# Kernel tuning notes

Hardware: AMD Instinct MI355X
Metric: run time of the kernel (lower is better)

## Reference

```python
import jax, jax.numpy as jnp
import numpy as np

NUM_SEGMENTS = 1024  # batch_size (graphs per batch)
NUM_HEADS = 4
HIDDEN = 64
INPUT_DIM = 512
NUM_NODES = 262144


def setup_inputs() -> dict:
    key = jax.random.key(0)
    ks = jax.random.split(key, 8)
    x = jax.random.normal(ks[0], (NUM_NODES, INPUT_DIM), dtype=jnp.float32)
    batch = jnp.sort(jax.random.randint(ks[1], (NUM_NODES,), 0, NUM_SEGMENTS)).astype(jnp.int64)
    # per-head attention projection weights/biases (torch Linear: y = x @ W.T + b)
    Wh = jax.random.normal(ks[2], (NUM_HEADS, HIDDEN, INPUT_DIM), dtype=jnp.float32) * 0.05
    bh = jnp.zeros((NUM_HEADS, HIDDEN), dtype=jnp.float32)
    ctx = jax.random.normal(ks[3], (NUM_HEADS, HIDDEN), dtype=jnp.float32) * 0.1
    Wc = jax.random.normal(ks[4], (INPUT_DIM, NUM_HEADS * INPUT_DIM), dtype=jnp.float32) * 0.02
    bc = jnp.zeros((INPUT_DIM,), dtype=jnp.float32)
    return {"x": x, "batch": batch, "Wh": Wh, "bh": bh, "ctx": ctx, "Wc": Wc, "bc": bc}


def _segment_softmax(scores, batch, num_segments):
    # scores: [N, H]; softmax over nodes within each graph segment, per head
    seg_max = jax.ops.segment_max(scores, batch, num_segments=num_segments)  # [B, H]
    shifted = jnp.exp(scores - seg_max[batch])                               # [N, H]
    seg_sum = jax.ops.segment_sum(shifted, batch, num_segments=num_segments)  # [B, H]
    return shifted / seg_sum[batch]


def reference(x, batch, Wh, bh, ctx, Wc, bc):
    batch = batch.astype(jnp.int32)
    # all heads at once: logits [N, H, K]
    logits = jnp.einsum('nd,hkd->nhk', x, Wh) + bh
    scores = jnp.einsum('nhk,hk->nh', jnp.tanh(logits), ctx)   # [N, H]
    weights = _segment_softmax(scores, batch, NUM_SEGMENTS)     # [N, H]
    weighted = weights[:, :, None] * x[:, None, :]              # [N, H, D]
    pooled = jax.ops.segment_sum(weighted, batch, num_segments=NUM_SEGMENTS)  # [B, H, D]
    concatenated = pooled.reshape(NUM_SEGMENTS, NUM_HEADS * INPUT_DIM)  # head0|head1|... order
    return concatenated @ Wc.T + bc
```

## Files before the change

### kernel.cpp

```cpp
#include <hip/hip_runtime.h>

#define NNODES 262144
#define NSEG   1024
#define DIN    512
#define NB     32
#define NBLK   (NNODES / NB)

typedef __attribute__((ext_vector_type(8))) short bf16x8;
typedef __attribute__((ext_vector_type(4))) float f32x4;

__device__ __forceinline__ unsigned short f2bf(float f){
  unsigned u = __float_as_uint(f);
  u += 0x7FFFu + ((u >> 16) & 1u);
  return (unsigned short)(u >> 16);
}

__device__ __forceinline__ float tanh_fast(float v){
  float z = fminf(fmaxf(v, -15.f), 15.f);
  float e = __expf(2.f * z);
  return (e - 1.f) / (e + 1.f);
}

__device__ __forceinline__ void atomic_addf(float* p, float v){
  __hip_atomic_fetch_add(p, v, __ATOMIC_RELAXED, __HIP_MEMORY_SCOPE_AGENT);
}

__global__ __launch_bounds__(256)
void k_prep(const float* __restrict__ wh, const float* __restrict__ wc,
            unsigned short* __restrict__ wbt, float* __restrict__ wct,
            float4* __restrict__ pooled4, float4* __restrict__ zsum4){
  int g = blockIdx.x * 256 + threadIdx.x;
  if (g < 131072){
    int ks = g >> 13, rem = g & 8191, hk = rem >> 5, kl = rem & 31;
    wbt[g] = f2bf(wh[hk * DIN + ks * 32 + kl]);
  } else if (g < 131072 + 1048576){
    int g2 = g - 131072;
    int j = g2 >> 9, o = g2 & 511;
    wct[g2] = wc[o * 2048 + j];
  } else if (g < 131072 + 1048576 + 524288){
    pooled4[g - 131072 - 1048576] = (float4){0.f, 0.f, 0.f, 0.f};
  } else if (g < 131072 + 1048576 + 524288 + 1024){
    zsum4[g - 131072 - 1048576 - 524288] = (float4){0.f, 0.f, 0.f, 0.f};
  }
}

__global__ __launch_bounds__(256)
void k_main(const float* __restrict__ x, const unsigned short* __restrict__ wbt,
            const float* __restrict__ bh, const float* __restrict__ ctx,
            const int* __restrict__ batch, float* __restrict__ pooled,
            float* __restrict__ zsum){
  __shared__ __align__(16) unsigned short xs[NB * DIN];
  __shared__ __align__(16) float wl[NB][4];
  __shared__ int bcache[NB];
  const int t = threadIdx.x, w = t >> 6, l = t & 63;
  const int nb = blockIdx.x * NB;

  const float4* xp = (const float4*)(x + (size_t)nb * DIN);
#pragma unroll 4
  for (int i = 0; i < 16; ++i){
    float4 v = xp[i * 256 + t];
    int flat = i * 1024 + t * 4;
    int row = flat >> 9, col = flat & 511;
    unsigned lo = (unsigned)f2bf(v.x) | ((unsigned)f2bf(v.y) << 16);
    unsigned hi = (unsigned)f2bf(v.z) | ((unsigned)f2bf(v.w) << 16);
    int byte = (row << 10) + (col << 1);
    byte ^= (row & 7) << 4;
    *(uint2*)((char*)xs + byte) = make_uint2(lo, hi);
  }
  if (t < NB) bcache[t] = batch[nb + t];

  float bhv[4], cxv[4];
#pragma unroll
  for (int q = 0; q < 4; ++q){
    int hk = (w * 4 + q) * 16 + (l & 15);
    bhv[q] = bh[hk];
    cxv[q] = ctx[hk];
  }

  bf16x8 Ba[4], Bb[4];
#pragma unroll
  for (int q = 0; q < 4; ++q)
    Ba[q] = *(const bf16x8*)(wbt + ((w * 4 + q) * 16 + (l & 15)) * 32 + (l >> 4) * 8);

  f32x4 acc[2][4];
#pragma unroll
  for (int nt = 0; nt < 2; ++nt)
#pragma unroll
    for (int q = 0; q < 4; ++q) acc[nt][q] = (f32x4){0.f, 0.f, 0.f, 0.f};

  __syncthreads();

  const int fr  = (l & 15);
  const int fcb = (l >> 4) * 16;
#pragma unroll
  for (int ks2 = 0; ks2 < 16; ks2 += 2){
    {
      const unsigned short* wp = wbt + (ks2 + 1) * 8192;
#pragma unroll
      for (int q = 0; q < 4; ++q)
        Bb[q] = *(const bf16x8*)(wp + ((w * 4 + q) * 16 + fr) * 32 + (l >> 4) * 8);
    }
    {
      int b0 = (fr << 10) + (ks2 << 6) + fcb;        b0 ^= (fr & 7) << 4;
      int b1 = ((16 + fr) << 10) + (ks2 << 6) + fcb; b1 ^= (fr & 7) << 4;
      bf16x8 A0 = *(const bf16x8*)((const char*)xs + b0);
      bf16x8 A1 = *(const bf16x8*)((const char*)xs + b1);
#pragma unroll
      for (int q = 0; q < 4; ++q){
        acc[0][q] = __builtin_amdgcn_mfma_f32_16x16x32_bf16(A0, Ba[q], acc[0][q], 0, 0, 0);
        acc[1][q] = __builtin_amdgcn_mfma_f32_16x16x32_bf16(A1, Ba[q], acc[1][q], 0, 0, 0);
      }
    }
    if (ks2 + 2 < 16){
      const unsigned short* wp = wbt + (ks2 + 2) * 8192;
#pragma unroll
      for (int q = 0; q < 4; ++q)
        Ba[q] = *(const bf16x8*)(wp + ((w * 4 + q) * 16 + fr) * 32 + (l >> 4) * 8);
    }
    {
      int b0 = (fr << 10) + ((ks2 + 1) << 6) + fcb;        b0 ^= (fr & 7) << 4;
      int b1 = ((16 + fr) << 10) + ((ks2 + 1) << 6) + fcb; b1 ^= (fr & 7) << 4;
      bf16x8 A0 = *(const bf16x8*)((const char*)xs + b0);
      bf16x8 A1 = *(const bf16x8*)((const char*)xs + b1);
#pragma unroll
      for (int q = 0; q < 4; ++q){
        acc[0][q] = __builtin_amdgcn_mfma_f32_16x16x32_bf16(A0, Bb[q], acc[0][q], 0, 0, 0);
        acc[1][q] = __builtin_amdgcn_mfma_f32_16x16x32_bf16(A1, Bb[q], acc[1][q], 0, 0, 0);
      }
    }
  }

#pragma unroll
  for (int r = 0; r < 4; ++r){
    float s0 = 0.f, s1 = 0.f;
#pragma unroll
    for (int q = 0; q < 4; ++q){
      s0 += tanh_fast(acc[0][q][r] + bhv[q]) * cxv[q];
      s1 += tanh_fast(acc[1][q][r] + bhv[q]) * cxv[q];
    }
#pragma unroll
    for (int off = 1; off < 16; off <<= 1){
      s0 += __shfl_xor(s0, off);
      s1 += __shfl_xor(s1, off);
    }
    if ((l & 15) == 0){
      int node0 = (l >> 4) * 4 + r;
      wl[node0][w]      = __expf(s0);
      wl[16 + node0][w] = __expf(s1);
    }
  }
  __syncthreads();

  float2 a0 = {0.f,0.f}, a1 = {0.f,0.f}, a2 = {0.f,0.f}, a3 = {0.f,0.f};
  int cur = bcache[0], run0 = 0;

#pragma unroll 4
  for (int n = 0; n < NB; ++n){
    int sg = bcache[n];
    if (sg != cur){
      float* base = pooled + (size_t)cur * 2048 + 2 * t;
      atomic_addf(base + 0,      a0.x); atomic_addf(base + 1,      a0.y);
      atomic_addf(base + 512,    a1.x); atomic_addf(base + 513,    a1.y);
      atomic_addf(base + 1024,   a2.x); atomic_addf(base + 1025,   a2.y);
      atomic_addf(base + 1536,   a3.x); atomic_addf(base + 1537,   a3.y);
      if (t < 4){
        float zs = 0.f;
        for (int m = run0; m < n; ++m) zs += wl[m][t];
        atomic_addf(zsum + cur * 4 + t, zs);
      }
      a0 = a1 = a2 = a3 = (float2){0.f, 0.f};
      cur = sg; run0 = n;
    }
    int byte = (n << 10) + (t << 2);
    byte ^= (n & 7) << 4;
    unsigned xv = *(const unsigned*)((const char*)xs + byte);
    float x0 = __uint_as_float(xv << 16);
    float x1 = __uint_as_float(xv & 0xFFFF0000u);
    float4 wv = *(const float4*)&wl[n][0];
    a0.x += wv.x * x0; a0.y += wv.x * x1;
    a1.x += wv.y * x0; a1.y += wv.y * x1;
    a2.x += wv.z * x0; a2.y += wv.z * x1;
    a3.x += wv.w * x0; a3.y += wv.w * x1;
  }
  {
    float* base = pooled + (size_t)cur * 2048 + 2 * t;
    atomic_addf(base + 0,      a0.x); atomic_addf(base + 1,      a0.y);
    atomic_addf(base + 512,    a1.x); atomic_addf(base + 513,    a1.y);
    atomic_addf(base + 1024,   a2.x); atomic_addf(base + 1025,   a2.y);
    atomic_addf(base + 1536,   a3.x); atomic_addf(base + 1537,   a3.y);
    if (t < 4){
      float zs = 0.f;
      for (int m = run0; m < NB; ++m) zs += wl[m][t];
      atomic_addf(zsum + cur * 4 + t, zs);
    }
  }
}

__global__ __launch_bounds__(256)
void k_out(const float* __restrict__ pooled, const float* __restrict__ wct,
           const float* __restrict__ zsum, const float* __restrict__ bias,
           float* __restrict__ out){
  __shared__ float ps[32][32];
  __shared__ float wt[32][64];
  __shared__ float rz[32][4];
  const int t = threadIdx.x;
  const int br = blockIdx.x >> 3, bc = blockIdx.x & 7;
  const int r0 = br * 32, c0 = bc * 64;
  if (t < 128){
    int row = t >> 2, h = t & 3;
    float z = zsum[(r0 + row) * 4 + h];
    rz[row][h] = (z > 0.f) ? 1.f / z : 0.f;
  }
  __syncthreads();

  const int w4 = t >> 6, col = t & 63;
  float acc[8];
#pragma unroll
  for (int i = 0; i < 8; ++i) acc[i] = 0.f;

  for (int j0 = 0; j0 < 2048; j0 += 32){
#pragma unroll
    for (int i = 0; i < 4; ++i){
      int e = i * 256 + t;
      int row = e >> 5, jj = e & 31;
      int j = j0 + jj;
      ps[row][jj] = pooled[(size_t)(r0 + row) * 2048 + j] * rz[row][j >> 9];
    }
#pragma unroll
    for (int i = 0; i < 8; ++i){
      int e = i * 256 + t;
      int jr = e >> 6, cc = e & 63;
      wt[jr][cc] = wct[(size_t)(j0 + jr) * 512 + c0 + cc];
    }
    __syncthreads();
#pragma unroll 8
    for (int jj = 0; jj < 32; ++jj){
      float wv = wt[jj][col];
#pragma unroll
      for (int i = 0; i < 8; ++i)
        acc[i] += ps[w4 * 8 + i][jj] * wv;
    }
    __syncthreads();
  }
  float bv = bias[c0 + col];
#pragma unroll
  for (int i = 0; i < 8; ++i)
    out[(size_t)(r0 + w4 * 8 + i) * 512 + c0 + col] = acc[i] + bv;
}

extern "C" void kernel_launch(void* const* d_in, const int* in_sizes, int n_in,
                              void* d_out, int out_size, void* d_ws, size_t ws_size,
                              hipStream_t stream){
  const float* x     = (const float*)d_in[0];
  const int*   batch = (const int*)d_in[1];
  const float* Wh    = (const float*)d_in[2];
  const float* bh    = (const float*)d_in[3];
  const float* ctx   = (const float*)d_in[4];
  const float* Wc    = (const float*)d_in[5];
  const float* bcv   = (const float*)d_in[6];
  float* out = (float*)d_out;

  char* ws = (char*)d_ws;
  unsigned short* wbt = (unsigned short*)(ws + 0);
  float* wct          = (float*)(ws + 262144);
  float* pooled       = (float*)(ws + 4456448);
  float* zsum         = (float*)(ws + 12845056);

  k_prep<<<6660, 256, 0, stream>>>(Wh, Wc, wbt, wct, (float4*)pooled, (float4*)zsum);
  k_main<<<NBLK, 256, 0, stream>>>(x, wbt, bh, ctx, batch, pooled, zsum);
  k_out <<<256, 256, 0, stream>>>(pooled, wct, zsum, bcv, out);
}
```

Baseline: 943.5 us.

## Double node tile per block, drop Wc transpose, shrink output tiles

```diff
diff --git a/kernel.cpp b/kernel.cpp
--- a/kernel.cpp
+++ b/kernel.cpp
@@ -3,7 +3,7 @@
 #define NNODES 262144
 #define NSEG   1024
 #define DIN    512
-#define NB     32
+#define NB     64
 #define NBLK   (NNODES / NB)
 
 typedef __attribute__((ext_vector_type(8))) short bf16x8;
@@ -26,21 +26,17 @@
 }
 
 __global__ __launch_bounds__(256)
-void k_prep(const float* __restrict__ wh, const float* __restrict__ wc,
-            unsigned short* __restrict__ wbt, float* __restrict__ wct,
+void k_prep(const float* __restrict__ wh,
+            unsigned short* __restrict__ wbt,
             float4* __restrict__ pooled4, float4* __restrict__ zsum4){
   int g = blockIdx.x * 256 + threadIdx.x;
   if (g < 131072){
     int ks = g >> 13, rem = g & 8191, hk = rem >> 5, kl = rem & 31;
     wbt[g] = f2bf(wh[hk * DIN + ks * 32 + kl]);
-  } else if (g < 131072 + 1048576){
-    int g2 = g - 131072;
-    int j = g2 >> 9, o = g2 & 511;
-    wct[g2] = wc[o * 2048 + j];
-  } else if (g < 131072 + 1048576 + 524288){
-    pooled4[g - 131072 - 1048576] = (float4){0.f, 0.f, 0.f, 0.f};
-  } else if (g < 131072 + 1048576 + 524288 + 1024){
-    zsum4[g - 131072 - 1048576 - 524288] = (float4){0.f, 0.f, 0.f, 0.f};
+  } else if (g < 131072 + 524288){
+    pooled4[g - 131072] = (float4){0.f, 0.f, 0.f, 0.f};
+  } else if (g < 131072 + 524288 + 1024){
+    zsum4[g - 131072 - 524288] = (float4){0.f, 0.f, 0.f, 0.f};
   }
 }
 
@@ -56,10 +52,10 @@
   const int nb = blockIdx.x * NB;
 
   const float4* xp = (const float4*)(x + (size_t)nb * DIN);
-#pragma unroll 4
-  for (int i = 0; i < 16; ++i){
+#pragma unroll 8
+  for (int i = 0; i < 32; ++i){
     float4 v = xp[i * 256 + t];
-    int flat = i * 1024 + t * 4;
+    int flat = (i * 256 + t) * 4;
     int row = flat >> 9, col = flat & 511;
     unsigned lo = (unsigned)f2bf(v.x) | ((unsigned)f2bf(v.y) << 16);
     unsigned hi = (unsigned)f2bf(v.z) | ((unsigned)f2bf(v.w) << 16);
@@ -69,10 +65,11 @@
   }
   if (t < NB) bcache[t] = batch[nb + t];
 
+  const int fr = l & 15, fc8 = (l >> 4) * 8;
   float bhv[4], cxv[4];
 #pragma unroll
   for (int q = 0; q < 4; ++q){
-    int hk = (w * 4 + q) * 16 + (l & 15);
+    int hk = (w * 4 + q) * 16 + fr;
     bhv[q] = bh[hk];
     cxv[q] = ctx[hk];
   }
@@ -80,17 +77,16 @@
   bf16x8 Ba[4], Bb[4];
 #pragma unroll
   for (int q = 0; q < 4; ++q)
-    Ba[q] = *(const bf16x8*)(wbt + ((w * 4 + q) * 16 + (l & 15)) * 32 + (l >> 4) * 8);
-
-  f32x4 acc[2][4];
-#pragma unroll
-  for (int nt = 0; nt < 2; ++nt)
+    Ba[q] = *(const bf16x8*)(wbt + ((w * 4 + q) * 16 + fr) * 32 + fc8);
+
+  f32x4 acc[4][4];
+#pragma unroll
+  for (int nt = 0; nt < 4; ++nt)
 #pragma unroll
     for (int q = 0; q < 4; ++q) acc[nt][q] = (f32x4){0.f, 0.f, 0.f, 0.f};
 
   __syncthreads();
 
-  const int fr  = (l & 15);
   const int fcb = (l >> 4) * 16;
 #pragma unroll
   for (int ks2 = 0; ks2 < 16; ks2 += 2){
@@ -98,55 +94,57 @@
       const unsigned short* wp = wbt + (ks2 + 1) * 8192;
 #pragma unroll
       for (int q = 0; q < 4; ++q)
-        Bb[q] = *(const bf16x8*)(wp + ((w * 4 + q) * 16 + fr) * 32 + (l >> 4) * 8);
+        Bb[q] = *(const bf16x8*)(wp + ((w * 4 + q) * 16 + fr) * 32 + fc8);
     }
     {
-      int b0 = (fr << 10) + (ks2 << 6) + fcb;        b0 ^= (fr & 7) << 4;
-      int b1 = ((16 + fr) << 10) + (ks2 << 6) + fcb; b1 ^= (fr & 7) << 4;
-      bf16x8 A0 = *(const bf16x8*)((const char*)xs + b0);
-      bf16x8 A1 = *(const bf16x8*)((const char*)xs + b1);
-#pragma unroll
-      for (int q = 0; q < 4; ++q){
-        acc[0][q] = __builtin_amdgcn_mfma_f32_16x16x32_bf16(A0, Ba[q], acc[0][q], 0, 0, 0);
-        acc[1][q] = __builtin_amdgcn_mfma_f32_16x16x32_bf16(A1, Ba[q], acc[1][q], 0, 0, 0);
+      bf16x8 A[4];
+#pragma unroll
+      for (int nt = 0; nt < 4; ++nt){
+        int b = ((nt * 16 + fr) << 10) + (ks2 << 6) + fcb;
+        b ^= (fr & 7) << 4;
+        A[nt] = *(const bf16x8*)((const char*)xs + b);
       }
+#pragma unroll
+      for (int nt = 0; nt < 4; ++nt)
+#pragma unroll
+        for (int q = 0; q < 4; ++q)
+          acc[nt][q] = __builtin_amdgcn_mfma_f32_16x16x32_bf16(A[nt], Ba[q], acc[nt][q], 0, 0, 0);
     }
     if (ks2 + 2 < 16){
       const unsigned short* wp = wbt + (ks2 + 2) * 8192;
 #pragma unroll
       for (int q = 0; q < 4; ++q)
-        Ba[q] = *(const bf16x8*)(wp + ((w * 4 + q) * 16 + fr) * 32 + (l >> 4) * 8);
+        Ba[q] = *(const bf16x8*)(wp + ((w * 4 + q) * 16 + fr) * 32 + fc8);
     }
     {
-      int b0 = (fr << 10) + ((ks2 + 1) << 6) + fcb;        b0 ^= (fr & 7) << 4;
-      int b1 = ((16 + fr) << 10) + ((ks2 + 1) << 6) + fcb; b1 ^= (fr & 7) << 4;
-      bf16x8 A0 = *(const bf16x8*)((const char*)xs + b0);
-      bf16x8 A1 = *(const bf16x8*)((const char*)xs + b1);
-#pragma unroll
-      for (int q = 0; q < 4; ++q){
-        acc[0][q] = __builtin_amdgcn_mfma_f32_16x16x32_bf16(A0, Bb[q], acc[0][q], 0, 0, 0);
-        acc[1][q] = __builtin_amdgcn_mfma_f32_16x16x32_bf16(A1, Bb[q], acc[1][q], 0, 0, 0);
+      bf16x8 A[4];
+#pragma unroll
+      for (int nt = 0; nt < 4; ++nt){
+        int b = ((nt * 16 + fr) << 10) + ((ks2 + 1) << 6) + fcb;
+        b ^= (fr & 7) << 4;
+        A[nt] = *(const bf16x8*)((const char*)xs + b);
       }
-    }
-  }
-
-#pragma unroll
-  for (int r = 0; r < 4; ++r){
-    float s0 = 0.f, s1 = 0.f;
-#pragma unroll
-    for (int q = 0; q < 4; ++q){
-      s0 += tanh_fast(acc[0][q][r] + bhv[q]) * cxv[q];
-      s1 += tanh_fast(acc[1][q][r] + bhv[q]) * cxv[q];
-    }
-#pragma unroll
-    for (int off = 1; off < 16; off <<= 1){
-      s0 += __shfl_xor(s0, off);
-      s1 += __shfl_xor(s1, off);
-    }
-    if ((l & 15) == 0){
-      int node0 = (l >> 4) * 4 + r;
-      wl[node0][w]      = __expf(s0);
-      wl[16 + node0][w] = __expf(s1);
+#pragma unroll
+      for (int nt = 0; nt < 4; ++nt)
+#pragma unroll
+        for (int q = 0; q < 4; ++q)
+          acc[nt][q] = __builtin_amdgcn_mfma_f32_16x16x32_bf16(A[nt], Bb[q], acc[nt][q], 0, 0, 0);
+    }
+  }
+
+#pragma unroll
+  for (int nt = 0; nt < 4; ++nt){
+#pragma unroll
+    for (int r = 0; r < 4; ++r){
+      float s = 0.f;
+#pragma unroll
+      for (int q = 0; q < 4; ++q)
+        s += tanh_fast(acc[nt][q][r] + bhv[q]) * cxv[q];
+#pragma unroll
+      for (int off = 1; off < 16; off <<= 1)
+        s += __shfl_xor(s, off);
+      if (fr == 0)
+        wl[nt * 16 + (l >> 4) * 4 + r][w] = __expf(s);
     }
   }
   __syncthreads();
@@ -154,7 +152,6 @@
   float2 a0 = {0.f,0.f}, a1 = {0.f,0.f}, a2 = {0.f,0.f}, a3 = {0.f,0.f};
   int cur = bcache[0], run0 = 0;
 
-#pragma unroll 4
   for (int n = 0; n < NB; ++n){
     int sg = bcache[n];
     if (sg != cur){
@@ -163,10 +160,13 @@
       atomic_addf(base + 512,    a1.x); atomic_addf(base + 513,    a1.y);
       atomic_addf(base + 1024,   a2.x); atomic_addf(base + 1025,   a2.y);
       atomic_addf(base + 1536,   a3.x); atomic_addf(base + 1537,   a3.y);
-      if (t < 4){
+      if (t < 64){
+        int h = t & 3, i0 = t >> 2;
         float zs = 0.f;
-        for (int m = run0; m < n; ++m) zs += wl[m][t];
-        atomic_addf(zsum + cur * 4 + t, zs);
+        for (int m = run0 + i0; m < n; m += 16) zs += wl[m][h];
+        zs += __shfl_xor(zs, 4);  zs += __shfl_xor(zs, 8);
+        zs += __shfl_xor(zs, 16); zs += __shfl_xor(zs, 32);
+        if (t < 4) atomic_addf(zsum + cur * 4 + t, zs);
       }
       a0 = a1 = a2 = a3 = (float2){0.f, 0.f};
       cur = sg; run0 = n;
@@ -188,25 +188,28 @@
     atomic_addf(base + 512,    a1.x); atomic_addf(base + 513,    a1.y);
     atomic_addf(base + 1024,   a2.x); atomic_addf(base + 1025,   a2.y);
     atomic_addf(base + 1536,   a3.x); atomic_addf(base + 1537,   a3.y);
-    if (t < 4){
+    if (t < 64){
+      int h = t & 3, i0 = t >> 2;
       float zs = 0.f;
-      for (int m = run0; m < NB; ++m) zs += wl[m][t];
-      atomic_addf(zsum + cur * 4 + t, zs);
+      for (int m = run0 + i0; m < NB; m += 16) zs += wl[m][h];
+      zs += __shfl_xor(zs, 4);  zs += __shfl_xor(zs, 8);
+      zs += __shfl_xor(zs, 16); zs += __shfl_xor(zs, 32);
+      if (t < 4) atomic_addf(zsum + cur * 4 + t, zs);
     }
   }
 }
 
 __global__ __launch_bounds__(256)
-void k_out(const float* __restrict__ pooled, const float* __restrict__ wct,
+void k_out(const float* __restrict__ pooled, const float* __restrict__ wc,
            const float* __restrict__ zsum, const float* __restrict__ bias,
            float* __restrict__ out){
-  __shared__ float ps[32][32];
-  __shared__ float wt[32][64];
-  __shared__ float rz[32][4];
+  __shared__ float ps[16][32];
+  __shared__ float wt[32][65];
+  __shared__ float rz[16][4];
   const int t = threadIdx.x;
   const int br = blockIdx.x >> 3, bc = blockIdx.x & 7;
-  const int r0 = br * 32, c0 = bc * 64;
-  if (t < 128){
+  const int r0 = br * 16, c0 = bc * 64;
+  if (t < 64){
     int row = t >> 2, h = t & 3;
     float z = zsum[(r0 + row) * 4 + h];
     rz[row][h] = (z > 0.f) ? 1.f / z : 0.f;
@@ -214,38 +217,36 @@
   __syncthreads();
 
   const int w4 = t >> 6, col = t & 63;
-  float acc[8];
-#pragma unroll
-  for (int i = 0; i < 8; ++i) acc[i] = 0.f;
+  float acc[4] = {0.f, 0.f, 0.f, 0.f};
 
   for (int j0 = 0; j0 < 2048; j0 += 32){
-#pragma unroll
-    for (int i = 0; i < 4; ++i){
+    int h0 = j0 >> 9;
+#pragma unroll
+    for (int i = 0; i < 2; ++i){
       int e = i * 256 + t;
       int row = e >> 5, jj = e & 31;
-      int j = j0 + jj;
-      ps[row][jj] = pooled[(size_t)(r0 + row) * 2048 + j] * rz[row][j >> 9];
+      ps[row][jj] = pooled[(size_t)(r0 + row) * 2048 + j0 + jj] * rz[row][h0];
     }
 #pragma unroll
     for (int i = 0; i < 8; ++i){
       int e = i * 256 + t;
-      int jr = e >> 6, cc = e & 63;
-      wt[jr][cc] = wct[(size_t)(j0 + jr) * 512 + c0 + cc];
+      int jj = e & 31, cc = e >> 5;
+      wt[jj][cc] = wc[(size_t)(c0 + cc) * 2048 + j0 + jj];
     }
     __syncthreads();
 #pragma unroll 8
     for (int jj = 0; jj < 32; ++jj){
       float wv = wt[jj][col];
 #pragma unroll
-      for (int i = 0; i < 8; ++i)
-        acc[i] += ps[w4 * 8 + i][jj] * wv;
+      for (int i = 0; i < 4; ++i)
+        acc[i] += ps[w4 * 4 + i][jj] * wv;
     }
     __syncthreads();
   }
   float bv = bias[c0 + col];
 #pragma unroll
-  for (int i = 0; i < 8; ++i)
-    out[(size_t)(r0 + w4 * 8 + i) * 512 + c0 + col] = acc[i] + bv;
+  for (int i = 0; i < 4; ++i)
+    out[(size_t)(r0 + w4 * 4 + i) * 512 + c0 + col] = acc[i] + bv;
 }
 
 extern "C" void kernel_launch(void* const* d_in, const int* in_sizes, int n_in,
@@ -262,11 +263,10 @@
 
   char* ws = (char*)d_ws;
   unsigned short* wbt = (unsigned short*)(ws + 0);
-  float* wct          = (float*)(ws + 262144);
-  float* pooled       = (float*)(ws + 4456448);
-  float* zsum         = (float*)(ws + 12845056);
-
-  k_prep<<<6660, 256, 0, stream>>>(Wh, Wc, wbt, wct, (float4*)pooled, (float4*)zsum);
+  float* pooled       = (float*)(ws + 262144);
+  float* zsum         = (float*)(ws + 8650752);
+
+  k_prep<<<2564, 256, 0, stream>>>(Wh, wbt, (float4*)pooled, (float4*)zsum);
   k_main<<<NBLK, 256, 0, stream>>>(x, wbt, bh, ctx, batch, pooled, zsum);
-  k_out <<<256, 256, 0, stream>>>(pooled, wct, zsum, bcv, out);
-}
+  k_out <<<512, 256, 0, stream>>>(pooled, Wc, zsum, bcv, out);
+}
```

After: 958.8 us. No clear change (+1.6%).
